# Kernel optimization log

Hardware: AMD Instinct MI355X
Metric: run time of the kernel (lower is better)

Reference implementation:

```python
import jax, jax.numpy as jnp
import numpy as np

C_IN = 128   # pair channel dim
H = 4        # heads
DH = 32      # per-head dim (c_hidden // no_heads = 128 // 4)
R = 96       # low-rank bias rank (hard-coded self.Rank)
N = 384      # sequence length (pair rep is N x N)
S_DIM = 449  # s_inputs feature dim (c_in + 449 into bias MLPs)
MLP_H = 256  # bias MLP hidden width
EPS = 1e-5


def setup_inputs() -> dict:
    key = jax.random.key(0)
    ks = jax.random.split(key, 16)
    w = lambda k, shp, s=0.02: (jax.random.normal(k, shp) * s).astype(jnp.float32)
    return {
        "x": jax.random.normal(ks[0], (N, N, C_IN), dtype=jnp.float32),
        "s_inputs": jax.random.normal(ks[1], (N, S_DIM), dtype=jnp.float32),
        "ln_gamma": jnp.ones((C_IN,), jnp.float32),
        "ln_beta": jnp.zeros((C_IN,), jnp.float32),
        # q flashbias MLP (Linear->Tanh->Linear->Tanh->Linear, no bias)
        "Wq1": w(ks[2], (C_IN + S_DIM, MLP_H)),
        "Wq2": w(ks[3], (MLP_H, MLP_H)),
        "Wq3": w(ks[4], (MLP_H, H * R)),
        # k flashbias MLP
        "Wk1": w(ks[5], (C_IN + S_DIM, MLP_H)),
        "Wk2": w(ks[6], (MLP_H, MLP_H)),
        "Wk3": w(ks[7], (MLP_H, H * R)),
        # OpenFold-style gated Attention params
        "Wq_att": w(ks[8], (C_IN, H * DH)),
        "Wk_att": w(ks[9], (C_IN, H * DH)),
        "Wv_att": w(ks[10], (C_IN, H * DH)),
        "Wg": w(ks[11], (C_IN, H * DH)),
        "bg": jnp.zeros((H * DH,), jnp.float32),
        "Wo": w(ks[12], (H * DH, C_IN)),
        "bo": jnp.zeros((C_IN,), jnp.float32),
        "id": 10,  # id < 16 -> low-rank flashbias path
    }


def _layer_norm(x, gamma, beta):
    mu = jnp.mean(x, axis=-1, keepdims=True)
    var = jnp.var(x, axis=-1, keepdims=True)
    return (x - mu) * jax.lax.rsqrt(var + EPS) * gamma + beta


def _bias_mlp(z, W1, W2, W3):
    # [N, C+449] -> [N, H*R] -> [1, H, N, R]
    h = jnp.tanh(jnp.tanh(z @ W1) @ W2) @ W3
    return jnp.transpose(h.reshape(N, H, R), (1, 0, 2))[None]


def reference(x, s_inputs, ln_gamma, ln_beta, Wq1, Wq2, Wq3, Wk1, Wk2, Wk3,
              Wq_att, Wk_att, Wv_att, Wg, bg, Wo, bo, id=10):
    # starting=True, eval mode, s_inputs given, id < 16 -> low-rank bias path
    x = _layer_norm(x, ln_gamma, ln_beta)                       # [N, N, C]

    # low-rank triangle-bias factors (shared across rows, broadcast over dim 0)
    q_bias = _bias_mlp(jnp.concatenate([x.mean(1), s_inputs], -1), Wq1, Wq2, Wq3)  # [1,H,N,R]
    k_bias = _bias_mlp(jnp.concatenate([x.mean(0), s_inputs], -1), Wk1, Wk2, Wk3)  # [1,H,N,R]

    # multi-head attention over the last sequence axis, per row
    def heads(z, W):  # [N, N, C] -> [N, H, N, DH]
        return jnp.transpose((z @ W).reshape(N, N, H, DH), (0, 2, 1, 3))

    q = heads(x, Wq_att) * (1.0 / np.sqrt(DH)).astype(np.float32)
    k = heads(x, Wk_att)
    v = heads(x, Wv_att)

    scores = jnp.einsum("ihqd,ihkd->ihqk", q, k)                # [N,H,N,N]
    scores = scores + jnp.einsum("bhqr,bhkr->bhqk", q_bias, k_bias)  # broadcast over rows
    a = jax.nn.softmax(scores, axis=-1)

    o = jnp.einsum("ihqk,ihkd->ihqd", a, v)                     # [N,H,N,DH]
    o = jnp.transpose(o, (0, 2, 1, 3)).reshape(N, N, H * DH)
    g = jax.nn.sigmoid(x @ Wg + bg)                              # gating
    out = (g * o) @ Wo + bo                                      # [N, N, C]
    return out
```

## Files before the change

kernel.cpp:

```cpp
#include <hip/hip_runtime.h>
#include <cstdint>
#include <cstddef>

typedef _Float16 f16;
typedef __attribute__((ext_vector_type(2))) _Float16 f16x2;
typedef __attribute__((ext_vector_type(4))) _Float16 f16x4;
typedef __attribute__((ext_vector_type(8))) _Float16 f16x8;
typedef __attribute__((ext_vector_type(4))) float f32x4;

#define MFMA_16x16x32(a,b,c) __builtin_amdgcn_mfma_f32_16x16x32_f16((a),(b),(c),0,0,0)
#define MFMA_16x16x16(a,b,c) __builtin_amdgcn_mfma_f32_16x16x16f16((a),(b),(c),0,0,0)

#define NSEQ 384
#define CIN 128
#define NH 4
#define DHD 32
#define RNK 96
#define SDIM 449
#define MHID 256
#define NN (NSEQ*NSEQ)
#define LOG2E 1.4426950408889634f

#define KPAD 608
#define ZSTR 616
#define HSTR 264
#define OFF_W1 0
#define SZ_W1 (MHID*KPAD)
#define OFF_W2 (2*SZ_W1)
#define SZ_W2 (MHID*MHID)
#define OFF_W3 (OFF_W2 + 2*SZ_W2)
#define SZ_W3 ((NH*RNK)*MHID)
#define WMLP_TOT (OFF_W3 + 2*SZ_W3)

__global__ __launch_bounds__(256) void k_convert(const float* __restrict__ Wq, const float* __restrict__ Wk,
    const float* __restrict__ Wv, const float* __restrict__ Wg, const float* __restrict__ Wo,
    f16* __restrict__ W4T, f16* __restrict__ WoT) {
  int idx = blockIdx.x*256 + threadIdx.x;
  int c = idx >> 7, kk = idx & 127;
  if (c < 512) {
    int mat = c >> 7, cc = c & 127;
    const float* src = mat==0 ? Wq : (mat==1 ? Wk : (mat==2 ? Wv : Wg));
    W4T[c*CIN + kk] = (f16)src[kk*CIN + cc];
  } else {
    int cc = c - 512;
    WoT[cc*CIN + kk] = (f16)Wo[kk*CIN + cc];
  }
}

__global__ __launch_bounds__(256) void k_convert2(const float* __restrict__ Wq1, const float* __restrict__ Wq2,
    const float* __restrict__ Wq3, const float* __restrict__ Wk1, const float* __restrict__ Wk2,
    const float* __restrict__ Wk3, f16* __restrict__ wmlp) {
  int idx = blockIdx.x*256 + threadIdx.x;
  float val;
  if (idx < OFF_W2) {
    int m = idx / SZ_W1, r = idx - m*SZ_W1;
    int c = r / KPAD, kk = r - c*KPAD;
    const float* src = m ? Wk1 : Wq1;
    val = (kk < SDIM + CIN) ? src[kk*MHID + c] : 0.f;
  } else if (idx < OFF_W3) {
    int r = idx - OFF_W2;
    int m = r >> 16, rr = r & 65535;
    int c = rr >> 8, kk = rr & 255;
    const float* src = m ? Wk2 : Wq2;
    val = src[kk*MHID + c];
  } else {
    int r = idx - OFF_W3;
    int m = r / SZ_W3, rr = r - m*SZ_W3;
    int c = rr >> 8, kk = rr & 255;
    const float* src = m ? Wk3 : Wq3;
    val = src[kk*(NH*RNK) + c];
  }
  wmlp[idx] = (f16)val;
}

__global__ __launch_bounds__(256) void k_ln(const float* __restrict__ x, const float* __restrict__ gamma,
    const float* __restrict__ beta, f16* __restrict__ xn, float* __restrict__ rowm) {
  int b = blockIdx.x;
  int i = b >> 2, jbase = (b & 3) * 96;
  int t = threadIdx.x, wave = t >> 6, lane = t & 63;
  int half = lane >> 5, l31 = lane & 31;
  int c0 = l31 * 4;
  __shared__ float racc[CIN];
  if (t < CIN) racc[t] = 0.f;
  float4 g4 = *(const float4*)&gamma[c0];
  float4 b4 = *(const float4*)&beta[c0];
  float a0=0,a1=0,a2=0,a3=0;
  __syncthreads();
  for (int it = 0; it < 12; ++it) {
    int j = jbase + it*8 + wave*2 + half;
    const float4 v = *(const float4*)&x[(size_t)(i*NSEQ + j)*CIN + c0];
    float s = (v.x+v.y)+(v.z+v.w);
    float ss = (v.x*v.x+v.y*v.y)+(v.z*v.z+v.w*v.w);
#pragma unroll
    for (int off = 16; off >= 1; off >>= 1) { s += __shfl_xor(s, off); ss += __shfl_xor(ss, off); }
    float mean = s * (1.0f/CIN);
    float var = ss * (1.0f/CIN) - mean*mean;
    float rs = rsqrtf(var + 1e-5f);
    float y0 = (v.x-mean)*rs*g4.x + b4.x;
    float y1 = (v.y-mean)*rs*g4.y + b4.y;
    float y2 = (v.z-mean)*rs*g4.z + b4.z;
    float y3 = (v.w-mean)*rs*g4.w + b4.w;
    f16x4 w; w[0]=(f16)y0; w[1]=(f16)y1; w[2]=(f16)y2; w[3]=(f16)y3;
    *(f16x4*)&xn[(size_t)(i*NSEQ + j)*CIN + c0] = w;
    a0+=y0; a1+=y1; a2+=y2; a3+=y3;
  }
  atomicAdd(&racc[c0], a0); atomicAdd(&racc[c0+1], a1);
  atomicAdd(&racc[c0+2], a2); atomicAdd(&racc[c0+3], a3);
  __syncthreads();
  if (t < CIN) atomicAdd(&rowm[i*CIN + t], racc[t] * (1.0f/NSEQ));
}

__global__ __launch_bounds__(256) void k_colmean(const f16* __restrict__ xn, float* __restrict__ colm) {
  int j = blockIdx.x; int t = threadIdx.x;
  int c = t & 127, half = t >> 7;
  float acc = 0.f;
  int i0 = half*192;
#pragma unroll 4
  for (int ii = i0; ii < i0 + 192; ++ii)
    acc += (float)xn[(size_t)(ii*NSEQ + j)*CIN + c];
  __shared__ float sb[256];
  sb[t] = acc;
  __syncthreads();
  if (t < 128) colm[j*CIN + t] = (sb[t] + sb[t+128]) * (1.0f/NSEQ);
}

__global__ __launch_bounds__(256) void k_mlp2(const float* __restrict__ rowm, const float* __restrict__ colm,
    const float* __restrict__ sinp, const f16* __restrict__ wmlp,
    float* __restrict__ qbT, float* __restrict__ kbT) {
  int b = blockIdx.x;
  bool isQ = b < 12;
  int r0 = (isQ ? b : b - 12) * 32;
  const float* mean = isQ ? rowm : colm;
  const f16* W1T = wmlp + (isQ ? 0 : SZ_W1);
  const f16* W2T = wmlp + OFF_W2 + (isQ ? 0 : SZ_W2);
  const f16* W3T = wmlp + OFF_W3 + (isQ ? 0 : SZ_W3);
  float* outp = isQ ? qbT : kbT;
  int t = threadIdx.x, wave = t >> 6, lane = t & 63;
  int l15 = lane & 15, quad = lane >> 4;
  int rt = wave & 1, ch = wave >> 1;

  __shared__ __align__(16) f16 z[32*ZSTR];
  __shared__ __align__(16) f16 hbuf[2][32*HSTR];

  for (int idx = t; idx < 32*KPAD; idx += 256) {
    int row = idx / KPAD, u = idx - row*KPAD;
    float v;
    if (u < CIN) v = mean[(r0+row)*CIN + u];
    else if (u < CIN + SDIM) v = sinp[(r0+row)*SDIM + (u - CIN)];
    else v = 0.f;
    z[row*ZSTR + u] = (f16)v;
  }
  __syncthreads();

  {
    f32x4 acc[8];
#pragma unroll
    for (int c = 0; c < 8; ++c) acc[c] = (f32x4){0,0,0,0};
    for (int ks = 0; ks < 19; ++ks) {
      f16x8 af = *(const f16x8*)&z[(rt*16 + l15)*ZSTR + ks*32 + quad*8];
#pragma unroll
      for (int c = 0; c < 8; ++c) {
        f16x8 bf = *(const f16x8*)&W1T[(size_t)((ch*8 + c)*16 + l15)*KPAD + ks*32 + quad*8];
        acc[c] = MFMA_16x16x32(af, bf, acc[c]);
      }
    }
#pragma unroll
    for (int c = 0; c < 8; ++c) {
      int col = (ch*8 + c)*16 + l15;
#pragma unroll
      for (int r = 0; r < 4; ++r) {
        float th = 1.f - 2.f/(1.f + __expf(2.f*acc[c][r]));
        hbuf[0][(rt*16 + quad*4 + r)*HSTR + col] = (f16)th;
      }
    }
  }
  __syncthreads();

  {
    f32x4 acc[8];
#pragma unroll
    for (int c = 0; c < 8; ++c) acc[c] = (f32x4){0,0,0,0};
    for (int ks = 0; ks < 8; ++ks) {
      f16x8 af = *(const f16x8*)&hbuf[0][(rt*16 + l15)*HSTR + ks*32 + quad*8];
#pragma unroll
      for (int c = 0; c < 8; ++c) {
        f16x8 bf = *(const f16x8*)&W2T[(size_t)((ch*8 + c)*16 + l15)*MHID + ks*32 + quad*8];
        acc[c] = MFMA_16x16x32(af, bf, acc[c]);
      }
    }
#pragma unroll
    for (int c = 0; c < 8; ++c) {
      int col = (ch*8 + c)*16 + l15;
#pragma unroll
      for (int r = 0; r < 4; ++r) {
        float th = 1.f - 2.f/(1.f + __expf(2.f*acc[c][r]));
        hbuf[1][(rt*16 + quad*4 + r)*HSTR + col] = (f16)th;
      }
    }
  }
  __syncthreads();

  {
    f32x4 acc[12];
#pragma unroll
    for (int c = 0; c < 12; ++c) acc[c] = (f32x4){0,0,0,0};
    for (int ks = 0; ks < 8; ++ks) {
      f16x8 af = *(const f16x8*)&hbuf[1][(rt*16 + l15)*HSTR + ks*32 + quad*8];
#pragma unroll
      for (int c = 0; c < 12; ++c) {
        f16x8 bf = *(const f16x8*)&W3T[(size_t)((ch*12 + c)*16 + l15)*MHID + ks*32 + quad*8];
        acc[c] = MFMA_16x16x32(af, bf, acc[c]);
      }
    }
#pragma unroll
    for (int c = 0; c < 12; ++c) {
      int o = (ch*12 + c)*16 + l15;
#pragma unroll
      for (int r = 0; r < 4; ++r)
        outp[o*NSEQ + r0 + rt*16 + quad*4 + r] = acc[c][r];
    }
  }
}

__global__ __launch_bounds__(128) void k_bias(const float* __restrict__ qbT, const float* __restrict__ kbT,
    float* __restrict__ bias4) {
  int b = blockIdx.x;
  int h = b / 96, kg = b - h*96;
  int t = threadIdx.x;
  __shared__ float4 kr[RNK];
  if (t < RNK) kr[t] = *(const float4*)&kbT[(size_t)(h*RNK + t)*NSEQ + kg*4];
  __syncthreads();
  float acc[3][4];
#pragma unroll
  for (int m = 0; m < 3; ++m)
#pragma unroll
    for (int r = 0; r < 4; ++r) acc[m][r] = 0.f;
  for (int r = 0; r < RNK; ++r) {
    float4 kv = kr[r];
    const float* qrow = qbT + (size_t)(h*RNK + r)*NSEQ;
    float q0 = qrow[t], q1 = qrow[t+128], q2 = qrow[t+256];
    acc[0][0]+=q0*kv.x; acc[0][1]+=q0*kv.y; acc[0][2]+=q0*kv.z; acc[0][3]+=q0*kv.w;
    acc[1][0]+=q1*kv.x; acc[1][1]+=q1*kv.y; acc[1][2]+=q1*kv.z; acc[1][3]+=q1*kv.w;
    acc[2][0]+=q2*kv.x; acc[2][1]+=q2*kv.y; acc[2][2]+=q2*kv.z; acc[2][3]+=q2*kv.w;
  }
#pragma unroll
  for (int m = 0; m < 3; ++m) {
    int q = t + m*128;
    f32x4 w; w[0]=acc[m][0]*LOG2E; w[1]=acc[m][1]*LOG2E; w[2]=acc[m][2]*LOG2E; w[3]=acc[m][3]*LOG2E;
    *(f32x4*)&bias4[((size_t)b*NSEQ + q)*4] = w;
  }
}

__global__ __launch_bounds__(256) void k_proj(const f16* __restrict__ xn, const f16* __restrict__ W4T,
    const float* __restrict__ bg, f16* __restrict__ qb, f16* __restrict__ kb, f16* __restrict__ vb,
    f16* __restrict__ gb) {
  int mb = blockIdx.x;
  int t = threadIdx.x, wave = t >> 6, lane = t & 63;
  int l15 = lane & 15, quad = lane >> 4;
  int m0 = wave*32;
  __shared__ __align__(16) f16 Bs[128*128];
  size_t grow = (size_t)mb*128 + m0;
  f16x8 af[2][4];
#pragma unroll
  for (int mt = 0; mt < 2; ++mt)
#pragma unroll
    for (int kt = 0; kt < 4; ++kt)
      af[mt][kt] = *(const f16x8*)&xn[(grow + mt*16 + l15)*CIN + (kt*4 + quad)*8];
  int i = mb/3, j0 = (mb - (mb/3)*3)*128 + m0;
  for (int nb = 0; nb < 4; ++nb) {
    for (int p = 0; p < 8; ++p) {
      int c = p*256 + t; int row = c >> 4, ci = c & 15;
      int sw = (ci ^ (row & 15)) * 8;
      *(f16x8*)&Bs[row*128 + sw] = *(const f16x8*)&W4T[(size_t)(nb*128 + row)*CIN + ci*8];
    }
    __syncthreads();
#pragma unroll
    for (int ct = 0; ct < 8; ++ct) {
      f32x4 acc0 = (f32x4){0,0,0,0}, acc1 = (f32x4){0,0,0,0};
#pragma unroll
      for (int kt = 0; kt < 4; ++kt) {
        f16x8 bf = *(const f16x8*)&Bs[(ct*16 + l15)*128 + ((kt*4 + quad) ^ l15)*8];
        acc0 = MFMA_16x16x32(af[0][kt], bf, acc0);
        acc1 = MFMA_16x16x32(af[1][kt], bf, acc1);
      }
      int col = nb*128 + ct*16 + l15;
      int cc = col & 127;
      int hh = cc >> 5, d = cc & 31;
      if (nb == 3) {
        float bgv = bg[cc];
#pragma unroll
        for (int mt = 0; mt < 2; ++mt) {
          f32x4 a = mt ? acc1 : acc0;
#pragma unroll
          for (int r = 0; r < 4; ++r) {
            int jj = j0 + mt*16 + quad*4 + r;
            float sg = 1.0f/(1.0f + __expf(-(a[r] + bgv)));
            gb[(size_t)(i*NSEQ + jj)*CIN + cc] = (f16)sg;
          }
        }
      } else {
        f16* dstb = nb==0 ? qb : (nb==1 ? kb : vb);
        float scale = nb==0 ? 0.25503576722f : 1.0f;
#pragma unroll
        for (int mt = 0; mt < 2; ++mt) {
          f32x4 a = mt ? acc1 : acc0;
#pragma unroll
          for (int r = 0; r < 4; ++r) {
            int jj = j0 + mt*16 + quad*4 + r;
            dstb[((size_t)(i*NH + hh)*NSEQ + jj)*DHD + d] = (f16)(a[r]*scale);
          }
        }
      }
    }
    __syncthreads();
  }
}

__global__ __launch_bounds__(256, 4) void k_attn(const f16* __restrict__ qg, const f16* __restrict__ kg,
    const f16* __restrict__ vg, const float* __restrict__ bias4, f16* __restrict__ og) {
  int b = blockIdx.x; int h = b / NSEQ; int i = b - h*NSEQ;
  int t = threadIdx.x; int wave = t >> 6; int lane = t & 63;
  int l15 = lane & 15, quad = lane >> 4;
  size_t base = (size_t)(i*NH + h) * NSEQ * DHD;
  int qt0 = wave*6;
  f16x8 qf[6];
#pragma unroll
  for (int s = 0; s < 6; ++s)
    qf[s] = *(const f16x8*)&qg[base + (size_t)((qt0+s)*16 + l15)*DHD + quad*8];
  f32x4 oa[6][2];
  float lsum[6];
#pragma unroll
  for (int s = 0; s < 6; ++s) { lsum[s] = 0.f; oa[s][0] = (f32x4){0,0,0,0}; oa[s][1] = (f32x4){0,0,0,0}; }
  const f16* kp = kg + base + (size_t)l15*DHD + quad*8;
  const f16* vp = vg + base + (size_t)(quad*4)*DHD + l15;
  const float* bp = bias4 + (((size_t)h*96 + quad)*NSEQ + qt0*16 + l15)*4;
  for (int kt = 0; kt < 24; ++kt) {
    f16x8 kf = *(const f16x8*)kp;
    f16x4 vf0, vf1;
#pragma unroll
    for (int jj = 0; jj < 4; ++jj) { vf0[jj] = vp[jj*DHD]; vf1[jj] = vp[jj*DHD + 16]; }
    f32x4 cb[6];
#pragma unroll
    for (int s = 0; s < 6; ++s) cb[s] = *(const f32x4*)(bp + s*64);
    kp += 16*DHD; vp += 16*DHD; bp += 4*NSEQ*4;
#pragma unroll
    for (int s = 0; s < 6; ++s) {
      f32x4 st = MFMA_16x16x32(kf, qf[s], cb[s]);
      float p0 = __builtin_amdgcn_exp2f(st[0]);
      float p1 = __builtin_amdgcn_exp2f(st[1]);
      float p2 = __builtin_amdgcn_exp2f(st[2]);
      float p3 = __builtin_amdgcn_exp2f(st[3]);
      lsum[s] += (p0 + p1) + (p2 + p3);
      f16x4 pa; pa[0]=(f16)p0; pa[1]=(f16)p1; pa[2]=(f16)p2; pa[3]=(f16)p3;
      oa[s][0] = MFMA_16x16x16(pa, vf0, oa[s][0]);
      oa[s][1] = MFMA_16x16x16(pa, vf1, oa[s][1]);
    }
  }
#pragma unroll
  for (int s = 0; s < 6; ++s) {
    float lf = lsum[s];
    lf += __shfl_xor(lf, 16);
    lf += __shfl_xor(lf, 32);
    float inv = 1.0f / lf;
#pragma unroll
    for (int r = 0; r < 4; ++r) {
      float invr = __shfl(inv, quad*4 + r);
      int qrow = (qt0+s)*16 + quad*4 + r;
      size_t ob = (size_t)(i*NSEQ + qrow)*(NH*DHD) + h*DHD;
      og[ob + l15]      = (f16)(oa[s][0][r] * invr);
      og[ob + 16 + l15] = (f16)(oa[s][1][r] * invr);
    }
  }
}

__global__ __launch_bounds__(256) void k_final(const f16* __restrict__ gb, const f16* __restrict__ ob,
    const f16* __restrict__ WoT, const float* __restrict__ bo, float* __restrict__ out) {
  int mb = blockIdx.x;
  int t = threadIdx.x, wave = t >> 6, lane = t & 63;
  int l15 = lane & 15, quad = lane >> 4;
  __shared__ __align__(16) f16 As[128*128];
  __shared__ __align__(16) f16 Bs[128*128];
  int Mbase = mb*128;
  for (int p = 0; p < 8; ++p) {
    int c = p*256 + t; int row = c >> 4, ci = c & 15;
    int sw = (ci ^ (row & 15)) * 8;
    f16x8 gv = *(const f16x8*)&gb[(size_t)(Mbase + row)*CIN + ci*8];
    f16x8 ov = *(const f16x8*)&ob[(size_t)(Mbase + row)*CIN + ci*8];
    *(f16x8*)&As[row*128 + sw] = gv*ov;
    *(f16x8*)&Bs[row*128 + sw] = *(const f16x8*)&WoT[row*CIN + ci*8];
  }
  __syncthreads();
  int m0 = wave*32;
  f16x8 af[2][4];
#pragma unroll
  for (int mt = 0; mt < 2; ++mt)
#pragma unroll
    for (int kt = 0; kt < 4; ++kt)
      af[mt][kt] = *(const f16x8*)&As[(m0 + mt*16 + l15)*128 + ((kt*4 + quad) ^ l15)*8];
#pragma unroll
  for (int ct = 0; ct < 8; ++ct) {
    f32x4 acc0 = (f32x4){0,0,0,0}, acc1 = (f32x4){0,0,0,0};
#pragma unroll
    for (int kt = 0; kt < 4; ++kt) {
      f16x8 bf = *(const f16x8*)&Bs[(ct*16 + l15)*128 + ((kt*4 + quad) ^ l15)*8];
      acc0 = MFMA_16x16x32(af[0][kt], bf, acc0);
      acc1 = MFMA_16x16x32(af[1][kt], bf, acc1);
    }
    float bov = bo[ct*16 + l15];
#pragma unroll
    for (int mt = 0; mt < 2; ++mt) {
      f32x4 a = mt ? acc1 : acc0;
#pragma unroll
      for (int r = 0; r < 4; ++r) {
        int mrow = Mbase + m0 + mt*16 + quad*4 + r;
        out[(size_t)mrow*CIN + ct*16 + l15] = a[r] + bov;
      }
    }
  }
}

extern "C" void kernel_launch(void* const* d_in, const int* in_sizes, int n_in,
                              void* d_out, int out_size, void* d_ws, size_t ws_size,
                              hipStream_t stream) {
  (void)in_sizes; (void)n_in; (void)out_size; (void)ws_size;
  const float* x    = (const float*)d_in[0];
  const float* sinp = (const float*)d_in[1];
  const float* gam  = (const float*)d_in[2];
  const float* bet  = (const float*)d_in[3];
  const float* Wq1  = (const float*)d_in[4];
  const float* Wq2  = (const float*)d_in[5];
  const float* Wq3  = (const float*)d_in[6];
  const float* Wk1  = (const float*)d_in[7];
  const float* Wk2  = (const float*)d_in[8];
  const float* Wk3  = (const float*)d_in[9];
  const float* Wqa  = (const float*)d_in[10];
  const float* Wka  = (const float*)d_in[11];
  const float* Wva  = (const float*)d_in[12];
  const float* Wg   = (const float*)d_in[13];
  const float* bg   = (const float*)d_in[14];
  const float* Wo   = (const float*)d_in[15];
  const float* bo   = (const float*)d_in[16];
  float* out = (float*)d_out;

  char* w = (char*)d_ws;
  auto carve = [&](size_t bytes) { char* p = w; w += (bytes + 255) & ~(size_t)255; return p; };
  f16*   xn    = (f16*)carve((size_t)NN*CIN*2);
  f16*   qb    = (f16*)carve((size_t)NN*CIN*2);
  f16*   kb    = (f16*)carve((size_t)NN*CIN*2);
  f16*   vb    = (f16*)carve((size_t)NN*CIN*2);
  f16*   gbuf  = (f16*)carve((size_t)NN*CIN*2);
  float* bias4 = (float*)carve((size_t)NH*NSEQ*NSEQ*4);
  float* rowm  = (float*)carve((size_t)NSEQ*CIN*4);
  float* colm  = (float*)carve((size_t)NSEQ*CIN*4);
  float* qbT   = (float*)carve((size_t)(NH*RNK)*NSEQ*4);
  float* kbT   = (float*)carve((size_t)(NH*RNK)*NSEQ*4);
  f16*   W4T   = (f16*)carve((size_t)512*CIN*2);
  f16*   WoT   = (f16*)carve((size_t)CIN*CIN*2);
  f16*   wmlp  = (f16*)carve((size_t)WMLP_TOT*2);
  f16*   obuf  = xn;

  hipMemsetAsync(rowm, 0, (size_t)NSEQ*CIN*4, stream);
  k_convert<<<320, 256, 0, stream>>>(Wqa, Wka, Wva, Wg, Wo, W4T, WoT);
  k_convert2<<<WMLP_TOT/256, 256, 0, stream>>>(Wq1, Wq2, Wq3, Wk1, Wk2, Wk3, wmlp);
  k_ln<<<NSEQ*4, 256, 0, stream>>>(x, gam, bet, xn, rowm);
  k_colmean<<<NSEQ, 256, 0, stream>>>(xn, colm);
  k_mlp2<<<24, 256, 0, stream>>>(rowm, colm, sinp, wmlp, qbT, kbT);
  k_bias<<<NH*96, 128, 0, stream>>>(qbT, kbT, bias4);
  k_proj<<<1152, 256, 0, stream>>>(xn, W4T, bg, qb, kb, vb, gbuf);
  k_attn<<<NH*NSEQ, 256, 0, stream>>>(qb, kb, vb, bias4, obuf);
  k_final<<<1152, 256, 0, stream>>>(gbuf, obuf, WoT, bo, out);
}
```

Before: 430.4 us.

## Transpose V layout and double-buffer K/V/bias loads in attention loop

The projection kernel now writes V transposed as [i,h,d,j], so the attention kernel can load each V fragment as a single f16x4 vector instead of four strided scalar loads. The attention inner loop also prefetches the next key tile's K, V and bias fragments into a second register buffer while computing the current tile. The launch-bounds occupancy hint drops from 4 to 3 blocks to leave room for the extra registers, which may lower the number of waves resident per CU.

```diff
diff --git a/kernel.cpp b/kernel.cpp
--- a/kernel.cpp
+++ b/kernel.cpp
@@ -298,8 +298,18 @@
             gb[(size_t)(i*NSEQ + jj)*CIN + cc] = (f16)sg;
           }
         }
+      } else if (nb == 2) {
+#pragma unroll
+        for (int mt = 0; mt < 2; ++mt) {
+          f32x4 a = mt ? acc1 : acc0;
+#pragma unroll
+          for (int r = 0; r < 4; ++r) {
+            int jj = j0 + mt*16 + quad*4 + r;
+            vb[((size_t)(i*NH + hh)*DHD + d)*NSEQ + jj] = (f16)a[r];
+          }
+        }
       } else {
-        f16* dstb = nb==0 ? qb : (nb==1 ? kb : vb);
+        f16* dstb = nb==0 ? qb : kb;
         float scale = nb==0 ? 0.25503576722f : 1.0f;
 #pragma unroll
         for (int mt = 0; mt < 2; ++mt) {
@@ -316,7 +326,16 @@
   }
 }
 
-__global__ __launch_bounds__(256, 4) void k_attn(const f16* __restrict__ qg, const f16* __restrict__ kg,
+#define ATTN_LOADSTEP(SLOT, KT) do {                                              \
+    kfb[SLOT] = *(const f16x8*)(kpl + (size_t)(KT)*16*DHD);                       \
+    v0b[SLOT] = *(const f16x4*)(vp0 + (KT)*16);                                   \
+    v1b[SLOT] = *(const f16x4*)(vp1 + (KT)*16);                                   \
+    const float* bq_ = bp + (size_t)(KT)*(4*NSEQ*4);                              \
+    _Pragma("unroll")                                                             \
+    for (int s_ = 0; s_ < 6; ++s_) cbb[SLOT][s_] = *(const f32x4*)(bq_ + s_*64);  \
+  } while (0)
+
+__global__ __launch_bounds__(256, 3) void k_attn(const f16* __restrict__ qg, const f16* __restrict__ kg,
     const f16* __restrict__ vg, const float* __restrict__ bias4, f16* __restrict__ og) {
   int b = blockIdx.x; int h = b / NSEQ; int i = b - h*NSEQ;
   int t = threadIdx.x; int wave = t >> 6; int lane = t & 63;
@@ -331,21 +350,23 @@
   float lsum[6];
 #pragma unroll
   for (int s = 0; s < 6; ++s) { lsum[s] = 0.f; oa[s][0] = (f32x4){0,0,0,0}; oa[s][1] = (f32x4){0,0,0,0}; }
-  const f16* kp = kg + base + (size_t)l15*DHD + quad*8;
-  const f16* vp = vg + base + (size_t)(quad*4)*DHD + l15;
+  const f16* kpl = kg + base + (size_t)l15*DHD + quad*8;
+  const f16* vt  = vg + base;
+  const f16* vp0 = vt + (size_t)l15*NSEQ + quad*4;
+  const f16* vp1 = vt + (size_t)(l15+16)*NSEQ + quad*4;
   const float* bp = bias4 + (((size_t)h*96 + quad)*NSEQ + qt0*16 + l15)*4;
+
+  f16x8 kfb[2]; f16x4 v0b[2], v1b[2]; f32x4 cbb[2][6];
+  ATTN_LOADSTEP(0, 0);
+#pragma unroll 2
   for (int kt = 0; kt < 24; ++kt) {
-    f16x8 kf = *(const f16x8*)kp;
-    f16x4 vf0, vf1;
-#pragma unroll
-    for (int jj = 0; jj < 4; ++jj) { vf0[jj] = vp[jj*DHD]; vf1[jj] = vp[jj*DHD + 16]; }
-    f32x4 cb[6];
-#pragma unroll
-    for (int s = 0; s < 6; ++s) cb[s] = *(const f32x4*)(bp + s*64);
-    kp += 16*DHD; vp += 16*DHD; bp += 4*NSEQ*4;
+    const int cur = kt & 1;
+    if (kt < 23) ATTN_LOADSTEP(cur^1, kt+1);
+    f16x8 kf = kfb[cur];
+    f16x4 vf0 = v0b[cur], vf1 = v1b[cur];
 #pragma unroll
     for (int s = 0; s < 6; ++s) {
-      f32x4 st = MFMA_16x16x32(kf, qf[s], cb[s]);
+      f32x4 st = MFMA_16x16x32(kf, qf[s], cbb[cur][s]);
       float p0 = __builtin_amdgcn_exp2f(st[0]);
       float p1 = __builtin_amdgcn_exp2f(st[1]);
       float p2 = __builtin_amdgcn_exp2f(st[2]);
```

After: 848.0 us. +97.0%, slower.

## Store V transposed for vector loads in attention; load final GEMM A-operand directly

Applied to the files above, without the earlier changes.

The projection kernel now writes V in a [row, head, d, seq] transposed layout, so the attention kernel can fetch each V fragment with a single 4-element vector load instead of four strided scalar loads. Separately, the final output GEMM drops the shared-memory staging of the gated A operand: each wave loads gate and attention output directly from global memory into registers and multiplies them there, which removes one LDS buffer and its write/read pass. The transposed V store from the projection kernel is scattered with stride NSEQ, which may make those writes less coalesced.

```diff
diff --git a/kernel.cpp b/kernel.cpp
--- a/kernel.cpp
+++ b/kernel.cpp
@@ -298,8 +298,18 @@
             gb[(size_t)(i*NSEQ + jj)*CIN + cc] = (f16)sg;
           }
         }
+      } else if (nb == 2) {
+#pragma unroll
+        for (int mt = 0; mt < 2; ++mt) {
+          f32x4 a = mt ? acc1 : acc0;
+#pragma unroll
+          for (int r = 0; r < 4; ++r) {
+            int jj = j0 + mt*16 + quad*4 + r;
+            vb[((size_t)(i*NH + hh)*DHD + d)*NSEQ + jj] = (f16)a[r];
+          }
+        }
       } else {
-        f16* dstb = nb==0 ? qb : (nb==1 ? kb : vb);
+        f16* dstb = nb==0 ? qb : kb;
         float scale = nb==0 ? 0.25503576722f : 1.0f;
 #pragma unroll
         for (int mt = 0; mt < 2; ++mt) {
@@ -331,18 +341,19 @@
   float lsum[6];
 #pragma unroll
   for (int s = 0; s < 6; ++s) { lsum[s] = 0.f; oa[s][0] = (f32x4){0,0,0,0}; oa[s][1] = (f32x4){0,0,0,0}; }
-  const f16* kp = kg + base + (size_t)l15*DHD + quad*8;
-  const f16* vp = vg + base + (size_t)(quad*4)*DHD + l15;
+  const f16* kp  = kg + base + (size_t)l15*DHD + quad*8;
+  const f16* vt  = vg + base;
+  const f16* vp0 = vt + (size_t)l15*NSEQ + quad*4;
+  const f16* vp1 = vt + (size_t)(l15+16)*NSEQ + quad*4;
   const float* bp = bias4 + (((size_t)h*96 + quad)*NSEQ + qt0*16 + l15)*4;
   for (int kt = 0; kt < 24; ++kt) {
     f16x8 kf = *(const f16x8*)kp;
-    f16x4 vf0, vf1;
-#pragma unroll
-    for (int jj = 0; jj < 4; ++jj) { vf0[jj] = vp[jj*DHD]; vf1[jj] = vp[jj*DHD + 16]; }
+    f16x4 vf0 = *(const f16x4*)(vp0 + kt*16);
+    f16x4 vf1 = *(const f16x4*)(vp1 + kt*16);
     f32x4 cb[6];
 #pragma unroll
     for (int s = 0; s < 6; ++s) cb[s] = *(const f32x4*)(bp + s*64);
-    kp += 16*DHD; vp += 16*DHD; bp += 4*NSEQ*4;
+    kp += 16*DHD; bp += 4*NSEQ*4;
 #pragma unroll
     for (int s = 0; s < 6; ++s) {
       f32x4 st = MFMA_16x16x32(kf, qf[s], cb[s]);
@@ -378,25 +389,25 @@
   int mb = blockIdx.x;
   int t = threadIdx.x, wave = t >> 6, lane = t & 63;
   int l15 = lane & 15, quad = lane >> 4;
-  __shared__ __align__(16) f16 As[128*128];
   __shared__ __align__(16) f16 Bs[128*128];
-  int Mbase = mb*128;
   for (int p = 0; p < 8; ++p) {
     int c = p*256 + t; int row = c >> 4, ci = c & 15;
     int sw = (ci ^ (row & 15)) * 8;
-    f16x8 gv = *(const f16x8*)&gb[(size_t)(Mbase + row)*CIN + ci*8];
-    f16x8 ov = *(const f16x8*)&ob[(size_t)(Mbase + row)*CIN + ci*8];
-    *(f16x8*)&As[row*128 + sw] = gv*ov;
     *(f16x8*)&Bs[row*128 + sw] = *(const f16x8*)&WoT[row*CIN + ci*8];
   }
-  __syncthreads();
   int m0 = wave*32;
+  size_t grow = (size_t)mb*128 + m0;
   f16x8 af[2][4];
 #pragma unroll
   for (int mt = 0; mt < 2; ++mt)
 #pragma unroll
-    for (int kt = 0; kt < 4; ++kt)
-      af[mt][kt] = *(const f16x8*)&As[(m0 + mt*16 + l15)*128 + ((kt*4 + quad) ^ l15)*8];
+    for (int kt = 0; kt < 4; ++kt) {
+      size_t off = (grow + mt*16 + l15)*CIN + (kt*4 + quad)*8;
+      f16x8 gv = *(const f16x8*)&gb[off];
+      f16x8 ov = *(const f16x8*)&ob[off];
+      af[mt][kt] = gv*ov;
+    }
+  __syncthreads();
 #pragma unroll
   for (int ct = 0; ct < 8; ++ct) {
     f32x4 acc0 = (f32x4){0,0,0,0}, acc1 = (f32x4){0,0,0,0};
@@ -412,7 +423,7 @@
       f32x4 a = mt ? acc1 : acc0;
 #pragma unroll
       for (int r = 0; r < 4; ++r) {
-        int mrow = Mbase + m0 + mt*16 + quad*4 + r;
+        int mrow = (int)(grow) + mt*16 + quad*4 + r;
         out[(size_t)mrow*CIN + ct*16 + l15] = a[r] + bov;
       }
     }
```

Result: slower. 446.9 us (+3.8%).
